# Kernel tuning notes

Measured on AMD Instinct MI355X. Metric: run time of the kernel, lower is better.

The kernel has to match this reference:

```python
import jax, jax.numpy as jnp
import numpy as np

B, D, H = 524288, 128, 64  # batch, input_dim, hidden_dim; mask_dim = transform_dim = D//2 = 64


def _mlp(x, Wh, bh, Wo, bo):
    """eqx.nn.MLP with depth=3: 3 hidden relu layers then linear out.
    x: [B, in]; Wh: [3, H, in/H]; bh: [3, H]; Wo: [out, H]; bo: [out]."""
    h = x
    for i in range(Wh.shape[0]):  # fixed small layer loop
        h = jax.nn.relu(h @ Wh[i].T + bh[i])
    return h @ Wo.T + bo


def setup_inputs() -> dict:
    key = jax.random.key(0)
    ks = jax.random.split(key, 9)
    m = D // 2
    s = 1.0 / np.sqrt(H)  # lecun-ish init scale
    inp = {"x": jax.random.normal(ks[0], (B, D), dtype=jnp.float32)}
    inp["cond_Wh"] = jax.random.normal(ks[1], (3, H, m), dtype=jnp.float32) * s
    inp["cond_bh"] = jnp.zeros((3, H), dtype=jnp.float32)
    inp["cond_Wo"] = jax.random.normal(ks[2], (D - m, H), dtype=jnp.float32) * s
    inp["cond_bo"] = jnp.zeros((D - m,), dtype=jnp.float32)
    inp["scale_Wh"] = jax.random.normal(ks[3], (3, H, m), dtype=jnp.float32) * s
    inp["scale_bh"] = jnp.zeros((3, H), dtype=jnp.float32)
    inp["scale_Wo"] = jax.random.normal(ks[4], (D - m, H), dtype=jnp.float32) * s
    inp["scale_bo"] = jnp.zeros((D - m,), dtype=jnp.float32)
    return inp


def reference(x, cond_Wh, cond_bh, cond_Wo, cond_bo,
              scale_Wh, scale_bh, scale_Wo, scale_bo):
    m = x.shape[-1] // 2
    # mask = [1]*m + [0]*(D-m) -> mask_idx = [:m], transform_idx = [m:] (static contiguous split)
    x_masked = x[..., :m]
    x_transform = x[..., m:]
    shift = _mlp(x_masked, cond_Wh, cond_bh, cond_Wo, cond_bo)        # [B, D-m]
    log_scale = _mlp(x_masked, scale_Wh, scale_bh, scale_Wo, scale_bo)  # [B, D-m]
    scale = jnp.exp(jnp.clip(log_scale, -5, 3))
    y_transform = x_transform * scale + shift
    y = jnp.concatenate([x_masked, y_transform], axis=-1)  # scatter back (contiguous)
    logdet = jnp.sum(log_scale, axis=-1)  # note: unclipped log_scale, as in original
    return y, logdet
```

## Files before the change

kernel.cpp:

```cpp
#include <hip/hip_runtime.h>
#include <cstdint>

typedef __attribute__((ext_vector_type(8))) _Float16 half8;
typedef __attribute__((ext_vector_type(4))) _Float16 half4;
typedef __attribute__((ext_vector_type(4))) float f32x4;

__global__ void prep_weights(const float* __restrict__ cWh, const float* __restrict__ cWo,
                             const float* __restrict__ sWh, const float* __restrict__ sWo,
                             _Float16* __restrict__ wf) {
    int t = blockIdx.x * 256 + threadIdx.x;
    int e    = t & 7;
    int mt   = (t >> 3) & 3;
    int lane = (t >> 5) & 63;
    int kp   = (t >> 11) & 1;
    int L    = (t >> 12) & 7;
    const float* src = (L < 3)  ? cWh + L * 4096
                     : (L == 3) ? cWo
                     : (L < 7)  ? sWh + (L - 4) * 4096
                     :            sWo;
    int m = mt * 16 + (lane & 15);
    int k = (2 * kp + (e >> 2)) * 16 + 4 * (lane >> 4) + (e & 3);
    float w = src[m * 64 + k];
    _Float16 hi = (_Float16)w;
    _Float16 lo = (_Float16)(w - (float)hi);
    int off = lane * 32 + mt * 8 + e;
    int fi = (L * 2 + kp) * 2;
    wf[fi * 2048 + off]       = hi;
    wf[(fi + 1) * 2048 + off] = lo;
}

template<bool RELU>
__device__ __forceinline__ half8 cvt_frag(f32x4 a, f32x4 b) {
    half8 r;
#pragma unroll
    for (int i = 0; i < 4; ++i) {
        float va = RELU ? fmaxf(a[i], 0.f) : a[i];
        float vb = RELU ? fmaxf(b[i], 0.f) : b[i];
        r[i]     = (_Float16)va;
        r[i + 4] = (_Float16)vb;
    }
    return r;
}

__device__ __forceinline__ void run_layer(const _Float16* __restrict__ wf, int Lid,
                                          const float* __restrict__ bias, int lane, int g4,
                                          const half8 B[2][4], f32x4 acc[4][4]) {
#pragma unroll
    for (int mt = 0; mt < 4; ++mt) {
        f32x4 bb = *(const f32x4*)(bias + mt * 16 + g4);
#pragma unroll
        for (int nt = 0; nt < 4; ++nt) acc[mt][nt] = bb;
    }
#pragma unroll
    for (int kp = 0; kp < 2; ++kp) {
        half8 Ah[4], Al[4];
        const _Float16* p = wf + (Lid * 2 + kp) * 4096 + lane * 32;
#pragma unroll
        for (int mt = 0; mt < 4; ++mt) {
            Ah[mt] = *(const half8*)(p + mt * 8);
            Al[mt] = *(const half8*)(p + 2048 + mt * 8);
        }
#pragma unroll
        for (int nt = 0; nt < 4; ++nt)
#pragma unroll
            for (int mt = 0; mt < 4; ++mt) {
                acc[mt][nt] = __builtin_amdgcn_mfma_f32_16x16x32_f16(Ah[mt], B[kp][nt], acc[mt][nt], 0, 0, 0);
                acc[mt][nt] = __builtin_amdgcn_mfma_f32_16x16x32_f16(Al[mt], B[kp][nt], acc[mt][nt], 0, 0, 0);
            }
    }
}

__device__ __forceinline__ void acc_to_B_relu(const f32x4 acc[4][4], half8 B[2][4]) {
#pragma unroll
    for (int kp = 0; kp < 2; ++kp)
#pragma unroll
        for (int nt = 0; nt < 4; ++nt)
            B[kp][nt] = cvt_frag<true>(acc[2 * kp][nt], acc[2 * kp + 1][nt]);
}

__global__ __launch_bounds__(64, 2)
void coupling_main(const float* __restrict__ x,
                   const float* __restrict__ cbh, const float* __restrict__ cbo,
                   const float* __restrict__ sbh, const float* __restrict__ sbo,
                   const _Float16* __restrict__ wf,
                   float* __restrict__ y, float* __restrict__ logdet) {
    __shared__ float xstage[4096];
    const int lane = threadIdx.x;
    const int c = lane & 15;
    const int g = lane >> 4;
    const int g4 = g * 4;
    const long row0 = (long)blockIdx.x * 64;
    const float* xr = x + (row0 + c) * 128 + g4;
    float* yr = y + (row0 + c) * 128 + g4;

    f32x4 xm[4][4];
#pragma unroll
    for (int nt = 0; nt < 4; ++nt)
#pragma unroll
        for (int kt = 0; kt < 4; ++kt)
            xm[nt][kt] = *(const f32x4*)(xr + nt * 2048 + kt * 16);

    {
        const int rr = lane >> 4;
        const int s  = lane & 15;
#pragma unroll
        for (int i = 0; i < 16; ++i) {
            const int r = i * 4 + rr;
            const int j = s ^ (r & 7);
            const float* src = x + (row0 + r) * 128 + 64 + j * 4;
            __builtin_amdgcn_global_load_lds(
                (const __attribute__((address_space(1))) void*)src,
                (__attribute__((address_space(3))) void*)(xstage + i * 256),
                16, 0, 0);
        }
    }

    half8 B0[2][4];
#pragma unroll
    for (int nt = 0; nt < 4; ++nt) {
#pragma unroll
        for (int kt = 0; kt < 4; ++kt)
            __builtin_nontemporal_store(xm[nt][kt], (f32x4*)(yr + nt * 2048 + kt * 16));
        B0[0][nt] = cvt_frag<false>(xm[nt][0], xm[nt][1]);
        B0[1][nt] = cvt_frag<false>(xm[nt][2], xm[nt][3]);
    }

    f32x4 acc[4][4];
    half8 B[2][4];

    run_layer(wf, 0, cbh,       lane, g4, B0, acc);
    acc_to_B_relu(acc, B);
    run_layer(wf, 1, cbh + 64,  lane, g4, B, acc);
    acc_to_B_relu(acc, B);
    run_layer(wf, 2, cbh + 128, lane, g4, B, acc);
    acc_to_B_relu(acc, B);
    run_layer(wf, 3, cbo,       lane, g4, B, acc);
    half4 shp[4][4];
#pragma unroll
    for (int mt = 0; mt < 4; ++mt)
#pragma unroll
        for (int nt = 0; nt < 4; ++nt) {
            half4 s;
#pragma unroll
            for (int i = 0; i < 4; ++i) s[i] = (_Float16)acc[mt][nt][i];
            shp[mt][nt] = s;
        }

    run_layer(wf, 4, sbh,       lane, g4, B0, acc);
    acc_to_B_relu(acc, B);
    run_layer(wf, 5, sbh + 64,  lane, g4, B, acc);
    acc_to_B_relu(acc, B);
    run_layer(wf, 6, sbh + 128, lane, g4, B, acc);
    acc_to_B_relu(acc, B);
    run_layer(wf, 7, sbo,       lane, g4, B, acc);

    asm volatile("s_waitcnt vmcnt(0)" ::: "memory");
    __builtin_amdgcn_sched_barrier(0);

    float pld0 = 0.f, pld1 = 0.f, pld2 = 0.f, pld3 = 0.f;
#pragma unroll
    for (int nt = 0; nt < 4; ++nt) {
        float psum = 0.f;
        const int r = nt * 16 + c;
#pragma unroll
        for (int mt = 0; mt < 4; ++mt) {
            f32x4 ls = acc[mt][nt];
            psum += ls[0] + ls[1] + ls[2] + ls[3];
            const int j = (mt * 4 + g) ^ (r & 7);
            f32x4 xt = *(const f32x4*)(xstage + r * 64 + j * 4);
            half4 sp = shp[mt][nt];
            f32x4 o;
#pragma unroll
            for (int i = 0; i < 4; ++i) {
                float cl = fminf(fmaxf(ls[i], -5.f), 3.f);
                o[i] = xt[i] * __expf(cl) + (float)sp[i];
            }
            __builtin_nontemporal_store(o, (f32x4*)(yr + nt * 2048 + 64 + mt * 16));
        }
        if (nt == 0) pld0 = psum; else if (nt == 1) pld1 = psum;
        else if (nt == 2) pld2 = psum; else pld3 = psum;
    }
#pragma unroll
    for (int nt = 0; nt < 4; ++nt) {
        float v = (nt == 0) ? pld0 : (nt == 1) ? pld1 : (nt == 2) ? pld2 : pld3;
        v += __shfl_xor(v, 16);
        v += __shfl_xor(v, 32);
        if ((lane >> 4) == 0) logdet[row0 + nt * 16 + c] = v;
    }
}

extern "C" void kernel_launch(void* const* d_in, const int* in_sizes, int n_in,
                              void* d_out, int out_size, void* d_ws, size_t ws_size,
                              hipStream_t stream) {
    const float* x   = (const float*)d_in[0];
    const float* cWh = (const float*)d_in[1];
    const float* cbh = (const float*)d_in[2];
    const float* cWo = (const float*)d_in[3];
    const float* cbo = (const float*)d_in[4];
    const float* sWh = (const float*)d_in[5];
    const float* sbh = (const float*)d_in[6];
    const float* sWo = (const float*)d_in[7];
    const float* sbo = (const float*)d_in[8];

    const int B = in_sizes[0] / 128;

    _Float16* wf = (_Float16*)d_ws;

    prep_weights<<<128, 256, 0, stream>>>(cWh, cWo, sWh, sWo, wf);

    float* y = (float*)d_out;
    float* logdet = y + (size_t)B * 128;
    coupling_main<<<B / 64, 64, 0, stream>>>(x, cbh, cbo, sbh, sbo, wf, y, logdet);
}
```

Baseline: 155.4 us.

## Double-buffer high-half weight fragments across MLP layers to overlap loads with MFMA

Splits the weight fragment loads into hi and lo halves. The hi fragments for the next layer are prefetched into an alternating register buffer while the current layer's MFMAs run, and the first two layers' hi weights are loaded before the x stores. The MFMA loop is restructured so all hi products run before all lo products. The goal is to hide global/L2 weight-load latency behind matrix work, at the cost of more VGPRs (two hi buffers plus lo), which could hurt occupancy under launch_bounds(64,2).

```diff
diff --git a/kernel.cpp b/kernel.cpp
--- a/kernel.cpp
+++ b/kernel.cpp
@@ -42,32 +42,53 @@
     return r;
 }
 
-__device__ __forceinline__ void run_layer(const _Float16* __restrict__ wf, int Lid,
-                                          const float* __restrict__ bias, int lane, int g4,
-                                          const half8 B[2][4], f32x4 acc[4][4]) {
+__device__ __forceinline__ void load_Ah(const _Float16* __restrict__ wf, int Lid, int lane,
+                                        half8 Ah[2][4]) {
+#pragma unroll
+    for (int kp = 0; kp < 2; ++kp) {
+        const _Float16* p = wf + (Lid * 2 + kp) * 4096 + lane * 32;
+#pragma unroll
+        for (int mt = 0; mt < 4; ++mt) Ah[kp][mt] = *(const half8*)(p + mt * 8);
+    }
+}
+__device__ __forceinline__ void load_Al(const _Float16* __restrict__ wf, int Lid, int lane,
+                                        half8 Al[2][4]) {
+#pragma unroll
+    for (int kp = 0; kp < 2; ++kp) {
+        const _Float16* p = wf + (Lid * 2 + kp) * 4096 + 2048 + lane * 32;
+#pragma unroll
+        for (int mt = 0; mt < 4; ++mt) Al[kp][mt] = *(const half8*)(p + mt * 8);
+    }
+}
+
+template<bool PREF>
+__device__ __forceinline__ void layer_body(const _Float16* __restrict__ wf, int curL, int nextL,
+                                           const float* __restrict__ bias, int lane, int g4,
+                                           const half8 AhC[2][4], half8 AhN[2][4],
+                                           const half8 B[2][4], f32x4 acc[4][4]) {
 #pragma unroll
     for (int mt = 0; mt < 4; ++mt) {
         f32x4 bb = *(const f32x4*)(bias + mt * 16 + g4);
 #pragma unroll
         for (int nt = 0; nt < 4; ++nt) acc[mt][nt] = bb;
     }
-#pragma unroll
-    for (int kp = 0; kp < 2; ++kp) {
-        half8 Ah[4], Al[4];
-        const _Float16* p = wf + (Lid * 2 + kp) * 4096 + lane * 32;
-#pragma unroll
-        for (int mt = 0; mt < 4; ++mt) {
-            Ah[mt] = *(const half8*)(p + mt * 8);
-            Al[mt] = *(const half8*)(p + 2048 + mt * 8);
-        }
+    half8 Al[2][4];
+    load_Al(wf, curL, lane, Al);
+#pragma unroll
+    for (int kp = 0; kp < 2; ++kp)
 #pragma unroll
         for (int nt = 0; nt < 4; ++nt)
 #pragma unroll
-            for (int mt = 0; mt < 4; ++mt) {
-                acc[mt][nt] = __builtin_amdgcn_mfma_f32_16x16x32_f16(Ah[mt], B[kp][nt], acc[mt][nt], 0, 0, 0);
-                acc[mt][nt] = __builtin_amdgcn_mfma_f32_16x16x32_f16(Al[mt], B[kp][nt], acc[mt][nt], 0, 0, 0);
-            }
-    }
+            for (int mt = 0; mt < 4; ++mt)
+                acc[mt][nt] = __builtin_amdgcn_mfma_f32_16x16x32_f16(AhC[kp][mt], B[kp][nt], acc[mt][nt], 0, 0, 0);
+    if (PREF) load_Ah(wf, nextL, lane, AhN);
+#pragma unroll
+    for (int kp = 0; kp < 2; ++kp)
+#pragma unroll
+        for (int nt = 0; nt < 4; ++nt)
+#pragma unroll
+            for (int mt = 0; mt < 4; ++mt)
+                acc[mt][nt] = __builtin_amdgcn_mfma_f32_16x16x32_f16(Al[kp][mt], B[kp][nt], acc[mt][nt], 0, 0, 0);
 }
 
 __device__ __forceinline__ void acc_to_B_relu(const f32x4 acc[4][4], half8 B[2][4]) {
@@ -93,6 +114,9 @@
     const float* xr = x + (row0 + c) * 128 + g4;
     float* yr = y + (row0 + c) * 128 + g4;
 
+    half8 AhA[2][4], AhB[2][4];
+    load_Ah(wf, 0, lane, AhA);
+
     f32x4 xm[4][4];
 #pragma unroll
     for (int nt = 0; nt < 4; ++nt)
@@ -118,23 +142,28 @@
     half8 B0[2][4];
 #pragma unroll
     for (int nt = 0; nt < 4; ++nt) {
+        B0[0][nt] = cvt_frag<false>(xm[nt][0], xm[nt][1]);
+        B0[1][nt] = cvt_frag<false>(xm[nt][2], xm[nt][3]);
+    }
+
+    load_Ah(wf, 1, lane, AhB);
+
+#pragma unroll
+    for (int nt = 0; nt < 4; ++nt)
 #pragma unroll
         for (int kt = 0; kt < 4; ++kt)
             __builtin_nontemporal_store(xm[nt][kt], (f32x4*)(yr + nt * 2048 + kt * 16));
-        B0[0][nt] = cvt_frag<false>(xm[nt][0], xm[nt][1]);
-        B0[1][nt] = cvt_frag<false>(xm[nt][2], xm[nt][3]);
-    }
 
     f32x4 acc[4][4];
     half8 B[2][4];
 
-    run_layer(wf, 0, cbh,       lane, g4, B0, acc);
-    acc_to_B_relu(acc, B);
-    run_layer(wf, 1, cbh + 64,  lane, g4, B, acc);
-    acc_to_B_relu(acc, B);
-    run_layer(wf, 2, cbh + 128, lane, g4, B, acc);
-    acc_to_B_relu(acc, B);
-    run_layer(wf, 3, cbo,       lane, g4, B, acc);
+    layer_body<false>(wf, 0, 0, cbh,       lane, g4, AhA, AhB, B0, acc);
+    acc_to_B_relu(acc, B);
+    layer_body<true >(wf, 1, 2, cbh + 64,  lane, g4, AhB, AhA, B, acc);
+    acc_to_B_relu(acc, B);
+    layer_body<true >(wf, 2, 3, cbh + 128, lane, g4, AhA, AhB, B, acc);
+    acc_to_B_relu(acc, B);
+    layer_body<true >(wf, 3, 4, cbo,       lane, g4, AhB, AhA, B, acc);
     half4 shp[4][4];
 #pragma unroll
     for (int mt = 0; mt < 4; ++mt)
@@ -146,13 +175,13 @@
             shp[mt][nt] = s;
         }
 
-    run_layer(wf, 4, sbh,       lane, g4, B0, acc);
-    acc_to_B_relu(acc, B);
-    run_layer(wf, 5, sbh + 64,  lane, g4, B, acc);
-    acc_to_B_relu(acc, B);
-    run_layer(wf, 6, sbh + 128, lane, g4, B, acc);
-    acc_to_B_relu(acc, B);
-    run_layer(wf, 7, sbo,       lane, g4, B, acc);
+    layer_body<true >(wf, 4, 5, sbh,       lane, g4, AhA, AhB, B0, acc);
+    acc_to_B_relu(acc, B);
+    layer_body<true >(wf, 5, 6, sbh + 64,  lane, g4, AhB, AhA, B, acc);
+    acc_to_B_relu(acc, B);
+    layer_body<true >(wf, 6, 7, sbh + 128, lane, g4, AhA, AhB, B, acc);
+    acc_to_B_relu(acc, B);
+    layer_body<false>(wf, 7, 7, sbo,       lane, g4, AhB, AhA, B, acc);
 
     asm volatile("s_waitcnt vmcnt(0)" ::: "memory");
     __builtin_amdgcn_sched_barrier(0);
```

New measurement: 221.7 us. 1.43x slower.

## Process four row tiles per block with software prefetch of next tile's input

Applied to the files above, without the earlier changes.

Each block now handles four consecutive 64-row tiles in a loop instead of one. While finishing the epilogue of the current tile, it loads the next tile's masked half into a second register set and issues the LDS DMA for its transform half, so memory latency overlaps with MFMA work. This costs a second 16-register input buffer and a quarter as many blocks, which may lower occupancy and latency hiding across waves. The LDS staging buffer is reused across tiles, relying on ordering between the LDS reads and the next DMA.

```diff
diff --git a/kernel.cpp b/kernel.cpp
--- a/kernel.cpp
+++ b/kernel.cpp
@@ -78,6 +78,127 @@
             B[kp][nt] = cvt_frag<true>(acc[2 * kp][nt], acc[2 * kp + 1][nt]);
 }
 
+__device__ __forceinline__ void issue_xt_dma(const float* __restrict__ x, long row0,
+                                             float* xstage, int lane) {
+    const int rr = lane >> 4;
+    const int s  = lane & 15;
+#pragma unroll
+    for (int i = 0; i < 16; ++i) {
+        const int r = i * 4 + rr;
+        const int j = s ^ (r & 7);
+        const float* src = x + (row0 + r) * 128 + 64 + j * 4;
+        __builtin_amdgcn_global_load_lds(
+            (const __attribute__((address_space(1))) void*)src,
+            (__attribute__((address_space(3))) void*)(xstage + i * 256),
+            16, 0, 0);
+    }
+}
+
+__device__ __forceinline__ void load_xm(const float* __restrict__ x, long row0,
+                                        int c, int g4, f32x4 (&xm)[4][4]) {
+    const float* xr = x + (row0 + c) * 128 + g4;
+#pragma unroll
+    for (int nt = 0; nt < 4; ++nt)
+#pragma unroll
+        for (int kt = 0; kt < 4; ++kt)
+            xm[nt][kt] = *(const f32x4*)(xr + nt * 2048 + kt * 16);
+}
+
+__device__ __forceinline__ void tile_body(
+        const float* __restrict__ x,
+        const float* __restrict__ cbh, const float* __restrict__ cbo,
+        const float* __restrict__ sbh, const float* __restrict__ sbo,
+        const _Float16* __restrict__ wf,
+        float* __restrict__ y, float* __restrict__ logdet,
+        float* xstage, long row0, int lane, int c, int g, int g4,
+        f32x4 (&xmc)[4][4], f32x4 (&xmn)[4][4], bool pref) {
+    const float* xr = x + (row0 + c) * 128 + g4;
+    float* yr = y + (row0 + c) * 128 + g4;
+
+    half8 B0[2][4];
+#pragma unroll
+    for (int nt = 0; nt < 4; ++nt) {
+#pragma unroll
+        for (int kt = 0; kt < 4; ++kt)
+            __builtin_nontemporal_store(xmc[nt][kt], (f32x4*)(yr + nt * 2048 + kt * 16));
+        B0[0][nt] = cvt_frag<false>(xmc[nt][0], xmc[nt][1]);
+        B0[1][nt] = cvt_frag<false>(xmc[nt][2], xmc[nt][3]);
+    }
+
+    f32x4 acc[4][4];
+    half8 B[2][4];
+
+    run_layer(wf, 0, cbh,       lane, g4, B0, acc);
+    acc_to_B_relu(acc, B);
+    run_layer(wf, 1, cbh + 64,  lane, g4, B, acc);
+    acc_to_B_relu(acc, B);
+    run_layer(wf, 2, cbh + 128, lane, g4, B, acc);
+    acc_to_B_relu(acc, B);
+    run_layer(wf, 3, cbo,       lane, g4, B, acc);
+    half4 shp[4][4];
+#pragma unroll
+    for (int mt = 0; mt < 4; ++mt)
+#pragma unroll
+        for (int nt = 0; nt < 4; ++nt) {
+            half4 s;
+#pragma unroll
+            for (int i = 0; i < 4; ++i) s[i] = (_Float16)acc[mt][nt][i];
+            shp[mt][nt] = s;
+        }
+
+    run_layer(wf, 4, sbh,       lane, g4, B0, acc);
+    acc_to_B_relu(acc, B);
+    run_layer(wf, 5, sbh + 64,  lane, g4, B, acc);
+    acc_to_B_relu(acc, B);
+    run_layer(wf, 6, sbh + 128, lane, g4, B, acc);
+    acc_to_B_relu(acc, B);
+    run_layer(wf, 7, sbo,       lane, g4, B, acc);
+
+    asm volatile("s_waitcnt vmcnt(0)" ::: "memory");
+    __builtin_amdgcn_sched_barrier(0);
+
+    if (pref) {
+        load_xm(x, row0 + 64, c, g4, xmn);
+        __builtin_amdgcn_sched_barrier(0);
+    }
+
+    float pld0 = 0.f, pld1 = 0.f, pld2 = 0.f, pld3 = 0.f;
+#pragma unroll
+    for (int nt = 0; nt < 4; ++nt) {
+        float psum = 0.f;
+        const int r = nt * 16 + c;
+#pragma unroll
+        for (int mt = 0; mt < 4; ++mt) {
+            f32x4 ls = acc[mt][nt];
+            psum += ls[0] + ls[1] + ls[2] + ls[3];
+            const int j = (mt * 4 + g) ^ (r & 7);
+            f32x4 xt = *(const f32x4*)(xstage + r * 64 + j * 4);
+            half4 sp = shp[mt][nt];
+            f32x4 o;
+#pragma unroll
+            for (int i = 0; i < 4; ++i) {
+                float cl = fminf(fmaxf(ls[i], -5.f), 3.f);
+                o[i] = xt[i] * __expf(cl) + (float)sp[i];
+            }
+            __builtin_nontemporal_store(o, (f32x4*)(yr + nt * 2048 + 64 + mt * 16));
+        }
+        if (nt == 0) pld0 = psum; else if (nt == 1) pld1 = psum;
+        else if (nt == 2) pld2 = psum; else pld3 = psum;
+    }
+#pragma unroll
+    for (int nt = 0; nt < 4; ++nt) {
+        float v = (nt == 0) ? pld0 : (nt == 1) ? pld1 : (nt == 2) ? pld2 : pld3;
+        v += __shfl_xor(v, 16);
+        v += __shfl_xor(v, 32);
+        if (g == 0) logdet[row0 + nt * 16 + c] = v;
+    }
+
+    if (pref) {
+        __builtin_amdgcn_sched_barrier(0);
+        issue_xt_dma(x, row0 + 64, xstage, lane);
+    }
+}
+
 __global__ __launch_bounds__(64, 2)
 void coupling_main(const float* __restrict__ x,
                    const float* __restrict__ cbh, const float* __restrict__ cbo,
@@ -89,103 +210,20 @@
     const int c = lane & 15;
     const int g = lane >> 4;
     const int g4 = g * 4;
-    const long row0 = (long)blockIdx.x * 64;
-    const float* xr = x + (row0 + c) * 128 + g4;
-    float* yr = y + (row0 + c) * 128 + g4;
-
-    f32x4 xm[4][4];
-#pragma unroll
-    for (int nt = 0; nt < 4; ++nt)
-#pragma unroll
-        for (int kt = 0; kt < 4; ++kt)
-            xm[nt][kt] = *(const f32x4*)(xr + nt * 2048 + kt * 16);
-
-    {
-        const int rr = lane >> 4;
-        const int s  = lane & 15;
-#pragma unroll
-        for (int i = 0; i < 16; ++i) {
-            const int r = i * 4 + rr;
-            const int j = s ^ (r & 7);
-            const float* src = x + (row0 + r) * 128 + 64 + j * 4;
-            __builtin_amdgcn_global_load_lds(
-                (const __attribute__((address_space(1))) void*)src,
-                (__attribute__((address_space(3))) void*)(xstage + i * 256),
-                16, 0, 0);
-        }
-    }
-
-    half8 B0[2][4];
-#pragma unroll
-    for (int nt = 0; nt < 4; ++nt) {
-#pragma unroll
-        for (int kt = 0; kt < 4; ++kt)
-            __builtin_nontemporal_store(xm[nt][kt], (f32x4*)(yr + nt * 2048 + kt * 16));
-        B0[0][nt] = cvt_frag<false>(xm[nt][0], xm[nt][1]);
-        B0[1][nt] = cvt_frag<false>(xm[nt][2], xm[nt][3]);
-    }
-
-    f32x4 acc[4][4];
-    half8 B[2][4];
-
-    run_layer(wf, 0, cbh,       lane, g4, B0, acc);
-    acc_to_B_relu(acc, B);
-    run_layer(wf, 1, cbh + 64,  lane, g4, B, acc);
-    acc_to_B_relu(acc, B);
-    run_layer(wf, 2, cbh + 128, lane, g4, B, acc);
-    acc_to_B_relu(acc, B);
-    run_layer(wf, 3, cbo,       lane, g4, B, acc);
-    half4 shp[4][4];
-#pragma unroll
-    for (int mt = 0; mt < 4; ++mt)
-#pragma unroll
-        for (int nt = 0; nt < 4; ++nt) {
-            half4 s;
-#pragma unroll
-            for (int i = 0; i < 4; ++i) s[i] = (_Float16)acc[mt][nt][i];
-            shp[mt][nt] = s;
-        }
-
-    run_layer(wf, 4, sbh,       lane, g4, B0, acc);
-    acc_to_B_relu(acc, B);
-    run_layer(wf, 5, sbh + 64,  lane, g4, B, acc);
-    acc_to_B_relu(acc, B);
-    run_layer(wf, 6, sbh + 128, lane, g4, B, acc);
-    acc_to_B_relu(acc, B);
-    run_layer(wf, 7, sbo,       lane, g4, B, acc);
-
-    asm volatile("s_waitcnt vmcnt(0)" ::: "memory");
-    __builtin_amdgcn_sched_barrier(0);
-
-    float pld0 = 0.f, pld1 = 0.f, pld2 = 0.f, pld3 = 0.f;
-#pragma unroll
-    for (int nt = 0; nt < 4; ++nt) {
-        float psum = 0.f;
-        const int r = nt * 16 + c;
-#pragma unroll
-        for (int mt = 0; mt < 4; ++mt) {
-            f32x4 ls = acc[mt][nt];
-            psum += ls[0] + ls[1] + ls[2] + ls[3];
-            const int j = (mt * 4 + g) ^ (r & 7);
-            f32x4 xt = *(const f32x4*)(xstage + r * 64 + j * 4);
-            half4 sp = shp[mt][nt];
-            f32x4 o;
-#pragma unroll
-            for (int i = 0; i < 4; ++i) {
-                float cl = fminf(fmaxf(ls[i], -5.f), 3.f);
-                o[i] = xt[i] * __expf(cl) + (float)sp[i];
-            }
-            __builtin_nontemporal_store(o, (f32x4*)(yr + nt * 2048 + 64 + mt * 16));
-        }
-        if (nt == 0) pld0 = psum; else if (nt == 1) pld1 = psum;
-        else if (nt == 2) pld2 = psum; else pld3 = psum;
-    }
-#pragma unroll
-    for (int nt = 0; nt < 4; ++nt) {
-        float v = (nt == 0) ? pld0 : (nt == 1) ? pld1 : (nt == 2) ? pld2 : pld3;
-        v += __shfl_xor(v, 16);
-        v += __shfl_xor(v, 32);
-        if ((lane >> 4) == 0) logdet[row0 + nt * 16 + c] = v;
+    const long base = (long)blockIdx.x * 256;
+
+    f32x4 xmA[4][4], xmB[4][4];
+
+    load_xm(x, base, c, g4, xmA);
+    issue_xt_dma(x, base, xstage, lane);
+
+#pragma unroll 1
+    for (int tt = 0; tt < 2; ++tt) {
+        const long r0 = base + (long)tt * 128;
+        tile_body(x, cbh, cbo, sbh, sbo, wf, y, logdet, xstage,
+                  r0,      lane, c, g, g4, xmA, xmB, true);
+        tile_body(x, cbh, cbo, sbh, sbo, wf, y, logdet, xstage,
+                  r0 + 64, lane, c, g, g4, xmB, xmA, tt == 0);
     }
 }
 
@@ -210,5 +248,5 @@
 
     float* y = (float*)d_out;
     float* logdet = y + (size_t)B * 128;
-    coupling_main<<<B / 64, 64, 0, stream>>>(x, cbh, cbo, sbh, sbo, wf, y, logdet);
-}
+    coupling_main<<<B / 256, 64, 0, stream>>>(x, cbh, cbo, sbh, sbo, wf, y, logdet);
+}
```

New measurement: 616.0 us. 296% more time.
